# Kernel optimization log

Measured on AMD Instinct MI355X. Metric: run time of the kernel, lower is better.

The kernel has to match this reference:

```python
import jax, jax.numpy as jnp
import numpy as np

N_NODES = 100000
N_EDGES = 1600000
D_IN = 32
D_OUT = 32


def setup_inputs() -> dict:
    key = jax.random.key(0)
    k1, k2, k3, k4 = jax.random.split(key, 4)
    edge_row = jax.random.randint(k1, (N_EDGES,), 0, N_NODES, dtype=jnp.int32)
    edge_col = jax.random.randint(k2, (N_EDGES,), 0, N_NODES, dtype=jnp.int32)
    edge_val = jnp.ones((N_EDGES,), dtype=jnp.float32)
    features = jax.random.normal(k3, (N_NODES, D_IN), dtype=jnp.float32)
    # torch nn.Linear weight layout: [out_dim, in_dim]
    W = jax.random.normal(k4, (D_OUT, D_IN), dtype=jnp.float32) * (1.0 / np.sqrt(D_IN))
    return {"edge_row": edge_row, "edge_col": edge_col, "edge_val": edge_val,
            "features": features, "W": W}


def reference(edge_row, edge_col, edge_val, features, W):
    n = features.shape[0]
    # degree = row-sums of A
    deg = jax.ops.segment_sum(edge_val, edge_row, num_segments=n)
    # D^{-1/2} with inf -> 0 (zero-degree nodes)
    d_inv_sqrt = jnp.where(deg > 0, jax.lax.rsqrt(deg), 0.0)
    # symmetric normalization on edge values: d^{-1/2}[r] * a * d^{-1/2}[c]
    vals = d_inv_sqrt[edge_row] * edge_val * d_inv_sqrt[edge_col]
    # SpMM: out[r] += vals * features[c]
    msgs = vals[:, None] * features[edge_col]  # [E, D_IN]
    agg = jax.ops.segment_sum(msgs, edge_row, num_segments=n)  # [N, D_IN]
    # linear (no bias), torch layout W: [out, in]
    return agg @ W.T
```

## Files before the change

### kernel.cpp

```cpp
#include <hip/hip_runtime.h>

#define D 32
#define CB 128
#define CAPC 2432
#define EPB 8192

__device__ __forceinline__ unsigned short f2bf(float f) {
    unsigned u = __float_as_uint(f);
    u += 0x7FFFu + ((u >> 16) & 1u);
    return (unsigned short)(u >> 16);
}
__device__ __forceinline__ float bf2f(unsigned short h) {
    return __uint_as_float(((unsigned)h) << 16);
}

__global__ void zero_kernel(int* __restrict__ gcount, int nb) {
    for (int t = threadIdx.x; t < nb; t += 512) gcount[t] = 0;
}

__global__ __launch_bounds__(512) void bucket_kernel(
        const int* __restrict__ row, const int* __restrict__ col,
        const float* __restrict__ val, int* __restrict__ gcount,
        int2* __restrict__ bkv, int E, int NBUCK) {
    __shared__ int hist[1024];
    __shared__ int base[1024];
    int t = threadIdx.x;
    for (int b = t; b < NBUCK; b += 512) hist[b] = 0;
    __syncthreads();
    long e0 = (long)blockIdx.x * EPB;
    int rr[16]; unsigned kk[16]; float vv[16];
#pragma unroll
    for (int u = 0; u < 4; ++u) {
        long e = e0 + (long)t * 4 + (long)u * 2048;
        if (e + 3 < E) {
            int4   r4 = *reinterpret_cast<const int4*>(&row[e]);
            int4   c4 = *reinterpret_cast<const int4*>(&col[e]);
            float4 v4 = *reinterpret_cast<const float4*>(&val[e]);
            rr[4*u+0] = r4.x; rr[4*u+1] = r4.y; rr[4*u+2] = r4.z; rr[4*u+3] = r4.w;
            kk[4*u+0] = ((unsigned)(r4.x & 127) << 17) | (unsigned)c4.x;
            kk[4*u+1] = ((unsigned)(r4.y & 127) << 17) | (unsigned)c4.y;
            kk[4*u+2] = ((unsigned)(r4.z & 127) << 17) | (unsigned)c4.z;
            kk[4*u+3] = ((unsigned)(r4.w & 127) << 17) | (unsigned)c4.w;
            vv[4*u+0] = v4.x; vv[4*u+1] = v4.y; vv[4*u+2] = v4.z; vv[4*u+3] = v4.w;
        } else {
#pragma unroll
            for (int k = 0; k < 4; ++k) {
                long ee = e + k;
                bool ok = ee < E;
                int r = ok ? row[ee] : -1;
                rr[4*u+k] = r;
                kk[4*u+k] = ok ? (((unsigned)(r & 127) << 17) | (unsigned)col[ee]) : 0u;
                vv[4*u+k] = ok ? val[ee] : 0.0f;
            }
        }
    }
#pragma unroll
    for (int i = 0; i < 16; ++i)
        if (rr[i] >= 0) atomicAdd(&hist[rr[i] >> 7], 1);
    __syncthreads();
    for (int b = t; b < NBUCK; b += 512) {
        int h = hist[b];
        base[b] = h ? atomicAdd(&gcount[b], h) : 0;
        hist[b] = 0;
    }
    __syncthreads();
#pragma unroll
    for (int i = 0; i < 16; ++i) {
        if (rr[i] >= 0) {
            int b = rr[i] >> 7;
            int rank = atomicAdd(&hist[b], 1);
            int pos = base[b] + rank;
            if (pos < CAPC)
                bkv[(long)b * CAPC + pos] = make_int2((int)kk[i], __float_as_int(vv[i]));
        }
    }
}

__global__ __launch_bounds__(256) void sortfine_kernel(
        const int* __restrict__ gcount, const int2* __restrict__ bkv,
        unsigned* __restrict__ cagg,
        int* __restrict__ rowstart, int* __restrict__ rowcnt,
        float* __restrict__ dis, int N) {
    __shared__ unsigned srt[CAPC];
    __shared__ int hist[CB], rs[CB], cur[CB];
    __shared__ float degl[CB];
    int t = threadIdx.x, b = blockIdx.x;
    if (t < CB) { hist[t] = 0; degl[t] = 0.0f; }
    __syncthreads();
    int n = gcount[b];
    if (n > CAPC) n = CAPC;
    long base = (long)b * CAPC;
    int2 kv[10]; bool ok[10];
#pragma unroll
    for (int u = 0; u < 10; ++u) {
        int idx = t + u * 256;
        ok[u] = idx < n;
        kv[u] = ok[u] ? bkv[base + idx] : make_int2(0, 0);
    }
#pragma unroll
    for (int u = 0; u < 10; ++u) {
        if (ok[u]) {
            int lr = ((unsigned)kv[u].x) >> 17;
            atomicAdd(&hist[lr], 1);
            atomicAdd(&degl[lr], __int_as_float(kv[u].y));
        }
    }
    __syncthreads();
    if (t < CB) rs[t] = hist[t];
    __syncthreads();
    for (int o = 1; o < CB; o <<= 1) {
        int v = (t < CB && t >= o) ? rs[t - o] : 0;
        __syncthreads();
        if (t < CB) rs[t] += v;
        __syncthreads();
    }
    if (t < CB) {
        int excl = rs[t] - hist[t];
        cur[t] = excl;
        int gr = (b << 7) + t;
        if (gr < N) {
            rowstart[gr] = (int)(base + excl);
            rowcnt[gr] = hist[t];
            float dg = degl[t];
            dis[gr] = dg > 0.0f ? rsqrtf(dg) : 0.0f;
        }
    }
    __syncthreads();
#pragma unroll
    for (int u = 0; u < 10; ++u) {
        if (ok[u]) {
            unsigned key = (unsigned)kv[u].x;
            int pos = atomicAdd(&cur[key >> 17], 1);
            srt[pos] = ((key & 0x1FFFFu) << 15) | (((unsigned)kv[u].y) >> 17);
        }
    }
    __syncthreads();
#pragma unroll
    for (int u = 0; u < 10; ++u) {
        int idx = t + u * 256;
        if (idx < n) cagg[base + idx] = srt[idx];
    }
}

__global__ void xw_kernel(const float* __restrict__ X, const float* __restrict__ W,
                          const float* __restrict__ dis,
                          unsigned short* __restrict__ Ybf, int N) {
    __shared__ float sWt[D][D + 1];
    __shared__ float sX[8][D];
    int t = threadIdx.x;
#pragma unroll
    for (int k = 0; k < 4; ++k) {
        int idx = t + k * 256;
        sWt[idx & 31][idx >> 5] = W[idx];
    }
    int r = t >> 5, c = t & 31;
    int n = blockIdx.x * 8 + r;
    if (n < N) sX[r][c] = X[n * D + c];
    __syncthreads();
    if (n < N) {
        float acc = 0.0f;
#pragma unroll
        for (int i = 0; i < D; ++i)
            acc += sX[r][i] * sWt[i][c];
        Ybf[(long)n * D + c] = f2bf(acc * dis[n]);
    }
}

__global__ __launch_bounds__(256) void agg_kernel(
        const int* __restrict__ rowstart, const int* __restrict__ rowcnt,
        const unsigned* __restrict__ cagg, const float* __restrict__ dis,
        const unsigned short* __restrict__ Ybf, float* __restrict__ out, int N) {
    int t = threadIdx.x;
    int wv = t >> 6, lane = t & 63;
    int sub = lane >> 3;
    int dl = lane & 7;
    int r0 = blockIdx.x * 16 + wv * 4;

    int st[4], cn[4];
    unsigned cr[4][3];
    ushort4 yv[4][3];
    float4 acc[4];
#pragma unroll
    for (int m = 0; m < 4; ++m) {
        int gr = r0 + m;
        bool v = gr < N;
        st[m] = v ? rowstart[gr] : 0;
        cn[m] = v ? rowcnt[gr] : 0;
        acc[m] = make_float4(0.f, 0.f, 0.f, 0.f);
    }
#pragma unroll
    for (int m = 0; m < 4; ++m) {
        int cm1 = cn[m] > 0 ? cn[m] - 1 : 0;
#pragma unroll
        for (int b = 0; b < 3; ++b) {
            int i = b * 8 + sub;
            cr[m][b] = cagg[st[m] + (i < cn[m] ? i : cm1)];
        }
    }
#pragma unroll
    for (int m = 0; m < 4; ++m)
#pragma unroll
        for (int b = 0; b < 3; ++b)
            yv[m][b] = *reinterpret_cast<const ushort4*>(
                &Ybf[(long)(cr[m][b] >> 15) * D + dl * 4]);
#pragma unroll
    for (int m = 0; m < 4; ++m) {
#pragma unroll
        for (int b = 0; b < 3; ++b) {
            int i = b * 8 + sub;
            float v = (i < cn[m]) ? __uint_as_float((cr[m][b] & 0x7FFFu) << 17) : 0.0f;
            acc[m].x = fmaf(v, bf2f(yv[m][b].x), acc[m].x);
            acc[m].y = fmaf(v, bf2f(yv[m][b].y), acc[m].y);
            acc[m].z = fmaf(v, bf2f(yv[m][b].z), acc[m].z);
            acc[m].w = fmaf(v, bf2f(yv[m][b].w), acc[m].w);
        }
    }
#pragma unroll
    for (int m = 0; m < 4; ++m) {
        for (int j = 24 + sub; j < cn[m]; j += 8) {
            unsigned c2 = cagg[st[m] + j];
            const ushort4 y2 = *reinterpret_cast<const ushort4*>(
                &Ybf[(long)(c2 >> 15) * D + dl * 4]);
            float v = __uint_as_float((c2 & 0x7FFFu) << 17);
            acc[m].x = fmaf(v, bf2f(y2.x), acc[m].x);
            acc[m].y = fmaf(v, bf2f(y2.y), acc[m].y);
            acc[m].z = fmaf(v, bf2f(y2.z), acc[m].z);
            acc[m].w = fmaf(v, bf2f(y2.w), acc[m].w);
        }
    }
#pragma unroll
    for (int m = 0; m < 4; ++m) {
#pragma unroll
        for (int s = 8; s <= 32; s <<= 1) {
            acc[m].x += __shfl_xor(acc[m].x, s, 64);
            acc[m].y += __shfl_xor(acc[m].y, s, 64);
            acc[m].z += __shfl_xor(acc[m].z, s, 64);
            acc[m].w += __shfl_xor(acc[m].w, s, 64);
        }
        int gr = r0 + m;
        if (gr < N && sub == 0) {
            float sc = dis[gr];
            *reinterpret_cast<float4*>(&out[(long)gr * D + dl * 4]) =
                make_float4(sc * acc[m].x, sc * acc[m].y, sc * acc[m].z, sc * acc[m].w);
        }
    }
}

extern "C" void kernel_launch(void* const* d_in, const int* in_sizes, int n_in,
                              void* d_out, int out_size, void* d_ws, size_t ws_size,
                              hipStream_t stream) {
    const int*   row = (const int*)d_in[0];
    const int*   col = (const int*)d_in[1];
    const float* val = (const float*)d_in[2];
    const float* X   = (const float*)d_in[3];
    const float* W   = (const float*)d_in[4];
    const int E = in_sizes[0];
    const int N = in_sizes[3] / D;
    float* out = (float*)d_out;

    const int NBUCK = (N + CB - 1) / CB;
    const size_t BKVSZ = (size_t)NBUCK * CAPC;

    char* w = (char*)d_ws;
    int*            gcount   = (int*)w;
    float*          dis      = (float*)(w + 16384);
    int*            rowstart = (int*)(w + 16384 + (size_t)N * 4);
    int*            rowcnt   = (int*)(w + 16384 + (size_t)N * 8);
    unsigned short* Ybf      = (unsigned short*)(w + 16384 + (size_t)N * 12);
    int2*           bkv      = (int2*)(w + 16384 + (size_t)N * 12 + (size_t)N * D * 2);
    unsigned*       cagg     = (unsigned*)((char*)bkv + BKVSZ * 8);

    zero_kernel<<<1, 512, 0, stream>>>(gcount, NBUCK);
    bucket_kernel<<<(E + EPB - 1) / EPB, 512, 0, stream>>>(
        row, col, val, gcount, bkv, E, NBUCK);
    sortfine_kernel<<<NBUCK, 256, 0, stream>>>(gcount, bkv, cagg,
                                               rowstart, rowcnt, dis, N);
    xw_kernel<<<(N + 7) / 8, 256, 0, stream>>>(X, W, dis, Ybf, N);
    agg_kernel<<<(N + 15) / 16, 256, 0, stream>>>(rowstart, rowcnt, cagg, dis, Ybf, out, N);
}
```

Baseline: 79.62 us.

## Use 512-row coarse buckets and scatter sorted edges directly to global

```diff
diff --git a/kernel.cpp b/kernel.cpp
--- a/kernel.cpp
+++ b/kernel.cpp
@@ -1,8 +1,8 @@
 #include <hip/hip_runtime.h>
 
 #define D 32
-#define CB 128
-#define CAPC 2432
+#define SB 512
+#define CAPSB 8704
 #define EPB 8192
 
 __device__ __forceinline__ unsigned short f2bf(float f) {
@@ -21,11 +21,11 @@
 __global__ __launch_bounds__(512) void bucket_kernel(
         const int* __restrict__ row, const int* __restrict__ col,
         const float* __restrict__ val, int* __restrict__ gcount,
-        int2* __restrict__ bkv, int E, int NBUCK) {
-    __shared__ int hist[1024];
-    __shared__ int base[1024];
+        int2* __restrict__ bkv, int E, int NSB) {
+    __shared__ int hist[256];
+    __shared__ int base[256];
     int t = threadIdx.x;
-    for (int b = t; b < NBUCK; b += 512) hist[b] = 0;
+    if (t < NSB) hist[t] = 0;
     __syncthreads();
     long e0 = (long)blockIdx.x * EPB;
     int rr[16]; unsigned kk[16]; float vv[16];
@@ -37,10 +37,10 @@
             int4   c4 = *reinterpret_cast<const int4*>(&col[e]);
             float4 v4 = *reinterpret_cast<const float4*>(&val[e]);
             rr[4*u+0] = r4.x; rr[4*u+1] = r4.y; rr[4*u+2] = r4.z; rr[4*u+3] = r4.w;
-            kk[4*u+0] = ((unsigned)(r4.x & 127) << 17) | (unsigned)c4.x;
-            kk[4*u+1] = ((unsigned)(r4.y & 127) << 17) | (unsigned)c4.y;
-            kk[4*u+2] = ((unsigned)(r4.z & 127) << 17) | (unsigned)c4.z;
-            kk[4*u+3] = ((unsigned)(r4.w & 127) << 17) | (unsigned)c4.w;
+            kk[4*u+0] = ((unsigned)(r4.x & 511) << 17) | (unsigned)c4.x;
+            kk[4*u+1] = ((unsigned)(r4.y & 511) << 17) | (unsigned)c4.y;
+            kk[4*u+2] = ((unsigned)(r4.z & 511) << 17) | (unsigned)c4.z;
+            kk[4*u+3] = ((unsigned)(r4.w & 511) << 17) | (unsigned)c4.w;
             vv[4*u+0] = v4.x; vv[4*u+1] = v4.y; vv[4*u+2] = v4.z; vv[4*u+3] = v4.w;
         } else {
 #pragma unroll
@@ -49,75 +49,65 @@
                 bool ok = ee < E;
                 int r = ok ? row[ee] : -1;
                 rr[4*u+k] = r;
-                kk[4*u+k] = ok ? (((unsigned)(r & 127) << 17) | (unsigned)col[ee]) : 0u;
+                kk[4*u+k] = ok ? (((unsigned)(r & 511) << 17) | (unsigned)col[ee]) : 0u;
                 vv[4*u+k] = ok ? val[ee] : 0.0f;
             }
         }
     }
 #pragma unroll
     for (int i = 0; i < 16; ++i)
-        if (rr[i] >= 0) atomicAdd(&hist[rr[i] >> 7], 1);
-    __syncthreads();
-    for (int b = t; b < NBUCK; b += 512) {
-        int h = hist[b];
-        base[b] = h ? atomicAdd(&gcount[b], h) : 0;
-        hist[b] = 0;
+        if (rr[i] >= 0) atomicAdd(&hist[rr[i] >> 9], 1);
+    __syncthreads();
+    if (t < NSB) {
+        int h = hist[t];
+        base[t] = h ? atomicAdd(&gcount[t], h) : 0;
+        hist[t] = 0;
     }
     __syncthreads();
 #pragma unroll
     for (int i = 0; i < 16; ++i) {
         if (rr[i] >= 0) {
-            int b = rr[i] >> 7;
+            int b = rr[i] >> 9;
             int rank = atomicAdd(&hist[b], 1);
             int pos = base[b] + rank;
-            if (pos < CAPC)
-                bkv[(long)b * CAPC + pos] = make_int2((int)kk[i], __float_as_int(vv[i]));
-        }
-    }
-}
-
-__global__ __launch_bounds__(256) void sortfine_kernel(
+            if (pos < CAPSB)
+                bkv[(long)b * CAPSB + pos] = make_int2((int)kk[i], __float_as_int(vv[i]));
+        }
+    }
+}
+
+__global__ __launch_bounds__(512) void sortfine_kernel(
         const int* __restrict__ gcount, const int2* __restrict__ bkv,
         unsigned* __restrict__ cagg,
         int* __restrict__ rowstart, int* __restrict__ rowcnt,
         float* __restrict__ dis, int N) {
-    __shared__ unsigned srt[CAPC];
-    __shared__ int hist[CB], rs[CB], cur[CB];
-    __shared__ float degl[CB];
+    __shared__ int hist[SB], rs[SB], cur[SB];
+    __shared__ float degl[SB];
     int t = threadIdx.x, b = blockIdx.x;
-    if (t < CB) { hist[t] = 0; degl[t] = 0.0f; }
+    hist[t] = 0; degl[t] = 0.0f;
     __syncthreads();
     int n = gcount[b];
-    if (n > CAPC) n = CAPC;
-    long base = (long)b * CAPC;
-    int2 kv[10]; bool ok[10];
-#pragma unroll
-    for (int u = 0; u < 10; ++u) {
-        int idx = t + u * 256;
-        ok[u] = idx < n;
-        kv[u] = ok[u] ? bkv[base + idx] : make_int2(0, 0);
-    }
-#pragma unroll
-    for (int u = 0; u < 10; ++u) {
-        if (ok[u]) {
-            int lr = ((unsigned)kv[u].x) >> 17;
-            atomicAdd(&hist[lr], 1);
-            atomicAdd(&degl[lr], __int_as_float(kv[u].y));
-        }
-    }
-    __syncthreads();
-    if (t < CB) rs[t] = hist[t];
-    __syncthreads();
-    for (int o = 1; o < CB; o <<= 1) {
-        int v = (t < CB && t >= o) ? rs[t - o] : 0;
+    if (n > CAPSB) n = CAPSB;
+    long base = (long)b * CAPSB;
+    for (int idx = t; idx < n; idx += 512) {
+        int2 kv = bkv[base + idx];
+        int lr = ((unsigned)kv.x) >> 17;
+        atomicAdd(&hist[lr], 1);
+        atomicAdd(&degl[lr], __int_as_float(kv.y));
+    }
+    __syncthreads();
+    rs[t] = hist[t];
+    __syncthreads();
+    for (int o = 1; o < SB; o <<= 1) {
+        int v = (t >= o) ? rs[t - o] : 0;
         __syncthreads();
-        if (t < CB) rs[t] += v;
+        rs[t] += v;
         __syncthreads();
     }
-    if (t < CB) {
+    {
         int excl = rs[t] - hist[t];
         cur[t] = excl;
-        int gr = (b << 7) + t;
+        int gr = (b << 9) + t;
         if (gr < N) {
             rowstart[gr] = (int)(base + excl);
             rowcnt[gr] = hist[t];
@@ -126,19 +116,11 @@
         }
     }
     __syncthreads();
-#pragma unroll
-    for (int u = 0; u < 10; ++u) {
-        if (ok[u]) {
-            unsigned key = (unsigned)kv[u].x;
-            int pos = atomicAdd(&cur[key >> 17], 1);
-            srt[pos] = ((key & 0x1FFFFu) << 15) | (((unsigned)kv[u].y) >> 17);
-        }
-    }
-    __syncthreads();
-#pragma unroll
-    for (int u = 0; u < 10; ++u) {
-        int idx = t + u * 256;
-        if (idx < n) cagg[base + idx] = srt[idx];
+    for (int idx = t; idx < n; idx += 512) {
+        int2 kv = bkv[base + idx];
+        unsigned key = (unsigned)kv.x;
+        int pos = atomicAdd(&cur[key >> 17], 1);
+        cagg[base + pos] = ((key & 0x1FFFFu) << 15) | (((unsigned)kv.y) >> 17);
     }
 }
 
@@ -258,8 +240,8 @@
     const int N = in_sizes[3] / D;
     float* out = (float*)d_out;
 
-    const int NBUCK = (N + CB - 1) / CB;
-    const size_t BKVSZ = (size_t)NBUCK * CAPC;
+    const int NSB = (N + SB - 1) / SB;
+    const size_t BKVSZ = (size_t)NSB * CAPSB;
 
     char* w = (char*)d_ws;
     int*            gcount   = (int*)w;
@@ -270,11 +252,11 @@
     int2*           bkv      = (int2*)(w + 16384 + (size_t)N * 12 + (size_t)N * D * 2);
     unsigned*       cagg     = (unsigned*)((char*)bkv + BKVSZ * 8);
 
-    zero_kernel<<<1, 512, 0, stream>>>(gcount, NBUCK);
+    zero_kernel<<<1, 512, 0, stream>>>(gcount, NSB);
     bucket_kernel<<<(E + EPB - 1) / EPB, 512, 0, stream>>>(
-        row, col, val, gcount, bkv, E, NBUCK);
-    sortfine_kernel<<<NBUCK, 256, 0, stream>>>(gcount, bkv, cagg,
-                                               rowstart, rowcnt, dis, N);
+        row, col, val, gcount, bkv, E, NSB);
+    sortfine_kernel<<<NSB, 512, 0, stream>>>(gcount, bkv, cagg,
+                                             rowstart, rowcnt, dis, N);
     xw_kernel<<<(N + 7) / 8, 256, 0, stream>>>(X, W, dis, Ybf, N);
     agg_kernel<<<(N + 15) / 16, 256, 0, stream>>>(rowstart, rowcnt, cagg, dis, Ybf, out, N);
 }
```

Measured after the change: 83.99 us. +5.5%, slower.
